# Kernel tuning notes

Hardware: AMD Instinct MI355X
Metric: run time of the kernel (lower is better)

The kernel has to match this reference:

```python
import jax, jax.numpy as jnp
import numpy as np

B, T, DIM, H, E, D, K = 2, 2048, 1024, 8, 5, 64, 3


def setup_inputs() -> dict:
    key = jax.random.key(0)
    ks = jax.random.split(key, 7)
    s = 0.02
    return {
        "x": jax.random.normal(ks[0], (B, T, DIM), dtype=jnp.float32),
        "w_q": jax.random.normal(ks[1], (DIM, H * E * D), dtype=jnp.float32) * s,
        "w_kv": jax.random.normal(ks[2], (DIM, 2 * H * E * D), dtype=jnp.float32) * s,
        "w_s": jax.random.normal(ks[3], (DIM, H * E), dtype=jnp.float32) * s,
        "w_d": jax.random.normal(ks[4], (DIM, H * E), dtype=jnp.float32) * s,
        "w_o_w": jax.random.normal(ks[5], (H, DIM, D), dtype=jnp.float32) * s,
        "w_o_b": jax.random.normal(ks[6], (H, DIM), dtype=jnp.float32) * s,
    }


def _select(proj_full, eps, s):
    # Faithful to torch scatter_(3, eps, s): value s[..., k] is written at
    # expert slot eps[..., k]; multiplying the full projection by that sparse
    # score tensor and summing over e == gather selected experts, weight by
    # the FIRST K raw scores (not the topk values), and sum.
    sel = jnp.take_along_axis(proj_full, eps[..., None], axis=3)  # b t h K d
    return (sel * s[..., :K, None]).sum(axis=3)  # b t h d


def reference(x, w_q, w_kv, w_s, w_d, w_o_w, w_o_b):
    scale = D ** (-0.5)
    ss = jax.nn.sigmoid(x @ w_s).reshape(B, T, H, E)
    sd = jax.nn.sigmoid(x @ w_d).reshape(B, T, H, E)
    eps_s = jax.lax.top_k(ss, K)[1]  # b t h K
    eps_d = jax.lax.top_k(sd, K)[1]

    q_full = (x @ w_q).reshape(B, T, H, E, D)
    q = _select(q_full, eps_d, sd)  # b t h d

    kv_full = (x @ w_kv).reshape(B, T, 2, H, E, D)
    k = _select(kv_full[:, :, 0], eps_s, ss)
    v = _select(kv_full[:, :, 1], eps_s, ss)

    attn = jnp.einsum("bihd,bjhd->bhij", q * scale, k)
    probs = jax.nn.softmax(attn, axis=-1)
    out = jnp.einsum("bhij,bjhd->bihd", probs, v)  # b t h d

    # per-head Linear(dim_head, dim) then sum over heads (stack+sum)
    return jnp.einsum("bihd,hfd->bif", out, w_o_w) + w_o_b.sum(axis=0)
```

## Files before the change

### kernel.cpp

```cpp
#include <hip/hip_runtime.h>

#define DEV __device__ __forceinline__

typedef float f32x4 __attribute__((ext_vector_type(4)));
typedef short s16x8 __attribute__((ext_vector_type(8)));
typedef unsigned short u16;
typedef unsigned int u32;

constexpr int Bb = 2, Tt = 2048, DIMc = 1024, Hh = 8, Ee = 5, Dd = 64;
constexpr int NTOK = Bb * Tt;
constexpr int NQ = Hh * Ee * Dd;

DEV u16 f2bf(float f) {
  union { float f; u32 u; } v; v.f = f;
  u32 r = v.u + 0x7fffu + ((v.u >> 16) & 1u);
  return (u16)(r >> 16);
}

DEV u32 pk2(float a, float b) {
  return (u32)f2bf(a) | ((u32)f2bf(b) << 16);
}

DEV s16x8 ld8(const u16* p) {
  uint4 u = *reinterpret_cast<const uint4*>(p);
  return __builtin_bit_cast(s16x8, u);
}

DEV f32x4 mfma16(s16x8 a, s16x8 b, f32x4 c) {
  return __builtin_amdgcn_mfma_f32_16x16x32_bf16(a, b, c, 0, 0, 0);
}

DEV void gld16(const void* g, void* l) {
  __builtin_amdgcn_global_load_lds(
      (const __attribute__((address_space(1))) void*)g,
      (__attribute__((address_space(3))) void*)l, 16, 0, 0);
}

__launch_bounds__(256)
__global__ void k_prep(const float* __restrict__ x, const float* __restrict__ wq,
                       const float* __restrict__ wkv, const float* __restrict__ wow,
                       const float* __restrict__ wob, const float* __restrict__ wsr,
                       const float* __restrict__ wdr,
                       u16* __restrict__ xb, u16* __restrict__ wT,
                       u16* __restrict__ woT, float* __restrict__ bsum,
                       float* __restrict__ wsdT) {
  int bid = blockIdx.x, t = threadIdx.x;
  if (bid < 4096) {
    int i = bid * 256 + t;
    float4 v = reinterpret_cast<const float4*>(x)[i];
    u16 r0 = f2bf(v.x), r1 = f2bf(v.y), r2 = f2bf(v.z), r3 = f2bf(v.w);
    u32 lo = (u32)r0 | ((u32)r1 << 16);
    u32 hi = (u32)r2 | ((u32)r3 << 16);
    reinterpret_cast<uint2*>(xb)[i] = make_uint2(lo, hi);
  } else if (bid < 11776) {
    int b2 = bid - 4096;
    int R0 = (b2 % 240) * 32;
    int C0 = (b2 / 240) * 32;
    int s = R0 / 2560, rem = R0 % 2560;
    int h = rem / 320, n0 = rem % 320;
    const float* src; int ld; int col0;
    if (s == 0) { src = wq;  ld = 2560; col0 = h * 320 + n0; }
    else        { src = wkv; ld = 5120; col0 = (s - 1) * 2560 + h * 320 + n0; }
    __shared__ float tile[32][33];
    int tx = t & 31, ty = t >> 5;
    #pragma unroll
    for (int i = 0; i < 4; i++) {
      int c = C0 + ty + 8 * i;
      tile[ty + 8 * i][tx] = src[(size_t)c * ld + col0 + tx];
    }
    __syncthreads();
    #pragma unroll
    for (int i = 0; i < 4; i++) {
      int n = ty + 8 * i;
      wT[(size_t)(R0 + n) * 1024 + C0 + tx] = f2bf(tile[tx][n]);
    }
  } else if (bid < 12032) {
    int b2 = bid - 11776;
    int f = b2 * 4 + (t >> 6), d = t & 63;
    #pragma unroll
    for (int h = 0; h < 8; h++)
      woT[(size_t)f * 512 + h * 64 + d] = f2bf(wow[((size_t)h * 1024 + f) * 64 + d]);
  } else if (bid < 12036) {
    int f = (bid - 12032) * 256 + t;
    float s = 0.f;
    #pragma unroll
    for (int h = 0; h < 8; h++) s += wob[h * 1024 + f];
    bsum[f] = s;
  } else {
    int j = bid - 12036;
    const float* src = (j < 40) ? wsr : wdr;
    int c = (j < 40) ? j : j - 40;
    for (int i = t; i < 1024; i += 256)
      wsdT[(size_t)j * 1024 + i] = src[(size_t)i * 40 + c];
  }
}

__launch_bounds__(320)
__global__ void k_scores(const float* __restrict__ x, const float* __restrict__ wsdT,
                         int* __restrict__ eps_s, int* __restrict__ eps_d,
                         float* __restrict__ ss3, float* __restrict__ sd3) {
  int tokb = blockIdx.x * 8;
  __shared__ float xl[8][1028];
  __shared__ float sc[8][80];
  const float4* xsrc = reinterpret_cast<const float4*>(x + (size_t)tokb * 1024);
  for (int i = threadIdx.x; i < 2048; i += 320) {
    int tok = i >> 8, col4 = i & 255;
    *reinterpret_cast<float4*>(&xl[tok][col4 * 4]) = xsrc[i];
  }
  __syncthreads();
  {
    int tok = threadIdx.x & 7, j = threadIdx.x >> 3;
    const float4* wsp = reinterpret_cast<const float4*>(wsdT + (size_t)j * 1024);
    const float4* wdp = reinterpret_cast<const float4*>(wsdT + (size_t)(j + 40) * 1024);
    float as0 = 0.f, as1 = 0.f, ad0 = 0.f, ad1 = 0.f;
    #pragma unroll 4
    for (int k4 = 0; k4 < 256; k4 += 2) {
      float4 x0 = *reinterpret_cast<const float4*>(&xl[tok][k4 * 4]);
      float4 x1 = *reinterpret_cast<const float4*>(&xl[tok][k4 * 4 + 4]);
      float4 wsv0 = wsp[k4], wsv1 = wsp[k4 + 1];
      float4 wdv0 = wdp[k4], wdv1 = wdp[k4 + 1];
      as0 += x0.x * wsv0.x + x0.y * wsv0.y + x0.z * wsv0.z + x0.w * wsv0.w;
      as1 += x1.x * wsv1.x + x1.y * wsv1.y + x1.z * wsv1.z + x1.w * wsv1.w;
      ad0 += x0.x * wdv0.x + x0.y * wdv0.y + x0.z * wdv0.z + x0.w * wdv0.w;
      ad1 += x1.x * wdv1.x + x1.y * wdv1.y + x1.z * wdv1.z + x1.w * wdv1.w;
    }
    float as = as0 + as1, ad = ad0 + ad1;
    sc[tok][j]      = 1.f / (1.f + expf(-as));
    sc[tok][40 + j] = 1.f / (1.f + expf(-ad));
  }
  __syncthreads();
  int t2 = threadIdx.x;
  if (t2 < 128) {
    int tt = t2 >> 4, u = t2 & 15, h = u >> 1, which = u & 1;
    const float* S = &sc[tt][which * 40 + h * 5];
    float v[5];
    #pragma unroll
    for (int e = 0; e < 5; e++) v[e] = S[e];
    int tok = tokb + tt;
    int base = (tok * 8 + h) * 3;
    int* eps = which ? eps_d : eps_s;
    float* w3 = which ? sd3 : ss3;
    bool used[5] = {false, false, false, false, false};
    #pragma unroll
    for (int kk = 0; kk < 3; kk++) {
      float best = -1e30f; int bi = 0;
      #pragma unroll
      for (int e = 0; e < 5; e++)
        if (!used[e] && v[e] > best) { best = v[e]; bi = e; }
      used[bi] = true;
      eps[base + kk] = bi;
    }
    #pragma unroll
    for (int kk = 0; kk < 3; kk++) w3[base + kk] = S[kk];
  }
}

__launch_bounds__(512)
__global__ void k_proj(const u16* __restrict__ xb, const u16* __restrict__ wT,
                       const int* __restrict__ eps_d, const int* __restrict__ eps_s,
                       const float* __restrict__ sd3, const float* __restrict__ ss3,
                       u16* __restrict__ qw, u16* __restrict__ kw, u16* __restrict__ vw) {
  int tok0 = blockIdx.x * 128;
  int h = blockIdx.y;
  int s = blockIdx.z;
  int Rbase = (s * 8 + h) * 320;
  __shared__ alignas(16) u16 bsA[128 * 64];
  __shared__ alignas(16) u16 bsB[320 * 64];
  int wv = threadIdx.x >> 6, l = threadIdx.x & 63;
  int g = l >> 4, c = l & 15;
  f32x4 acc[20];
  #pragma unroll
  for (int i = 0; i < 20; i++) acc[i] = (f32x4){0.f, 0.f, 0.f, 0.f};

  const u16* wTp0 = wT + (size_t)Rbase * 1024;
  const u16* xbp0 = xb + (size_t)tok0 * 1024;

  for (int k0 = 0; k0 < 1024; k0 += 64) {
    __syncthreads();
    const u16* wTp = wTp0 + k0;
    #pragma unroll
    for (int j = 0; j < 5; j++) {
      int ch = wv * 320 + j * 64 + l;
      int row = ch >> 3, part = ch & 7;
      gld16(wTp + (size_t)row * 1024 + ((part * 8) ^ ((row & 7) * 8)),
            &bsB[(wv * 320 + j * 64) * 8]);
    }
    const u16* xbp = xbp0 + k0;
    #pragma unroll
    for (int j = 0; j < 2; j++) {
      int ch = wv * 128 + j * 64 + l;
      int row = ch >> 3, part = ch & 7;
      gld16(xbp + (size_t)row * 1024 + ((part * 8) ^ ((row & 7) * 8)),
            &bsA[(wv * 128 + j * 64) * 8]);
    }
    __syncthreads();

    #pragma unroll
    for (int kk = 0; kk < 2; kk++) {
      int off = (kk * 32 + g * 8) ^ ((c & 7) * 8);
      s16x8 a = *reinterpret_cast<const s16x8*>(&bsA[(wv * 16 + c) * 64 + off]);
      #pragma unroll
      for (int nt = 0; nt < 20; nt++) {
        s16x8 b = *reinterpret_cast<const s16x8*>(&bsB[(nt * 16 + c) * 64 + off]);
        acc[nt] = mfma16(a, b, acc[nt]);
      }
    }
  }

  const int* eps = (s == 0) ? eps_d : eps_s;
  const float* w3 = (s == 0) ? sd3 : ss3;
  float scale = (s == 0) ? 0.125f : 1.0f;
  u16* dst = (s == 0) ? qw : (s == 1 ? kw : vw);
  #pragma unroll
  for (int r = 0; r < 4; r++) {
    int tokr = tok0 + wv * 16 + g * 4 + r;
    int base = (tokr * 8 + h) * 3;
    int e0 = eps[base], e1 = eps[base + 1], e2 = eps[base + 2];
    float w0 = w3[base], w1 = w3[base + 1], w2 = w3[base + 2];
    float we[5];
    #pragma unroll
    for (int e = 0; e < 5; e++)
      we[e] = (e0 == e ? w0 : 0.f) + (e1 == e ? w1 : 0.f) + (e2 == e ? w2 : 0.f);
    int b = tokr >> 11, t = tokr & 2047;
    size_t obase = (((size_t)b * 8 + h) * 2048 + t) * 64;
    #pragma unroll
    for (int dh = 0; dh < 4; dh++) {
      float vq = 0.f;
      #pragma unroll
      for (int e = 0; e < 5; e++) vq += we[e] * acc[e * 4 + dh][r];
      dst[obase + dh * 16 + c] = f2bf(vq * scale);
    }
  }
}

__global__ void k_trv(const u16* __restrict__ vw, u16* __restrict__ vT) {
  int bh = blockIdx.z;
  int t0 = blockIdx.x * 32, d0 = blockIdx.y * 32;
  __shared__ u16 tile[32][33];
  const u16* src = vw + (size_t)bh * 2048 * 64;
  u16* dst = vT + (size_t)bh * 64 * 2048;
  int tx = threadIdx.x, ty = threadIdx.y;
  #pragma unroll
  for (int i = 0; i < 4; i++)
    tile[ty + 8 * i][tx] = src[(size_t)(t0 + ty + 8 * i) * 64 + d0 + tx];
  __syncthreads();
  int p = 8 * ((tx & 15) >> 2) + (tx & 3) + ((tx >= 16) ? 4 : 0);
  #pragma unroll
  for (int i = 0; i < 4; i++)
    dst[(size_t)(d0 + ty + 8 * i) * 2048 + t0 + p] = tile[tx][ty + 8 * i];
}

__launch_bounds__(512)
__global__ void k_attn(const u16* __restrict__ qw, const u16* __restrict__ kw,
                       const u16* __restrict__ vT, u16* __restrict__ ow) {
  int bh = blockIdx.y;
  int b = bh >> 3, h = bh & 7;
  int q0 = blockIdx.x * 64;
  int wv = threadIdx.x >> 6, l = threadIdx.x & 63;
  int seg = wv >> 2, wq = wv & 3;
  int g = l >> 4, c = l & 15;
  const u16* qp = qw + (size_t)bh * 2048 * 64;
  const u16* kp = kw + (size_t)bh * 2048 * 64;
  const u16* vp = vT + (size_t)bh * 64 * 2048;
  __shared__ alignas(16) u16 Kl[2][128 * 64];
  __shared__ alignas(16) u16 Vl[2][64 * 128];

  s16x8 qa0 = ld8(qp + (size_t)(q0 + wq * 16 + c) * 64 + 0 + 8 * g);
  s16x8 qa1 = ld8(qp + (size_t)(q0 + wq * 16 + c) * 64 + 32 + 8 * g);

  f32x4 o[4];
  #pragma unroll
  for (int i = 0; i < 4; i++) o[i] = (f32x4){0.f, 0.f, 0.f, 0.f};
  float ssum = 0.f;

  const int kb0 = seg * 1024;
  for (int kt = 0; kt < 1024; kt += 128) {
    int kbase = kb0 + kt;
    __syncthreads();
    #pragma unroll
    for (int j = 0; j < 4; j++) {
      int ch = (wq * 4 + j) * 64 + l;
      int row = ch >> 3, sl = ch & 7;
      gld16(kp + (size_t)(kbase + row) * 64 + ((sl ^ (row & 7)) * 8),
            &Kl[seg][(wq * 4 + j) * 64 * 8]);
    }
    #pragma unroll
    for (int j = 0; j < 4; j++) {
      int ch = (wq * 4 + j) * 64 + l;
      int d = ch >> 4, sl = ch & 15;
      gld16(vp + (size_t)d * 2048 + kbase + ((sl ^ (d & 15)) * 8),
            &Vl[seg][(wq * 4 + j) * 64 * 8]);
    }
    __syncthreads();

    #pragma unroll
    for (int kk = 0; kk < 4; kk++) {
      int r0 = kk * 32 + c, r1 = kk * 32 + 16 + c;
      int c7 = c & 7;
      s16x8 ka0 = *reinterpret_cast<const s16x8*>(&Kl[seg][r0 * 64 + ((0 + g) ^ c7) * 8]);
      s16x8 ka1 = *reinterpret_cast<const s16x8*>(&Kl[seg][r0 * 64 + ((4 + g) ^ c7) * 8]);
      s16x8 kc0 = *reinterpret_cast<const s16x8*>(&Kl[seg][r1 * 64 + ((0 + g) ^ c7) * 8]);
      s16x8 kc1 = *reinterpret_cast<const s16x8*>(&Kl[seg][r1 * 64 + ((4 + g) ^ c7) * 8]);

      f32x4 s0 = (f32x4){0.f, 0.f, 0.f, 0.f};
      f32x4 s1 = (f32x4){0.f, 0.f, 0.f, 0.f};
      s0 = mfma16(ka0, qa0, s0);
      s0 = mfma16(ka1, qa1, s0);
      s1 = mfma16(kc0, qa0, s1);
      s1 = mfma16(kc1, qa1, s1);

      float p00 = __expf(s0[0]), p01 = __expf(s0[1]);
      float p02 = __expf(s0[2]), p03 = __expf(s0[3]);
      float p10 = __expf(s1[0]), p11 = __expf(s1[1]);
      float p12 = __expf(s1[2]), p13 = __expf(s1[3]);
      ssum += (p00 + p01) + (p02 + p03) + (p10 + p11) + (p12 + p13);

      uint4 pw = make_uint4(pk2(p00, p01), pk2(p02, p03),
                            pk2(p10, p11), pk2(p12, p13));
      s16x8 pa = __builtin_bit_cast(s16x8, pw);

      #pragma unroll
      for (int nt = 0; nt < 4; nt++) {
        int d = nt * 16 + c;
        s16x8 vb = *reinterpret_cast<const s16x8*>(&Vl[seg][d * 128 + (((kk * 4 + g) ^ (d & 15)) * 8)]);
        o[nt] = mfma16(pa, vb, o[nt]);
      }
    }
  }

  ssum += __shfl_xor(ssum, 16, 64);
  ssum += __shfl_xor(ssum, 32, 64);

  float* osp  = reinterpret_cast<float*>(&Kl[0][0]);
  float* sslp = reinterpret_cast<float*>(&Vl[0][0]);
  __syncthreads();
  if (g == 0) sslp[seg * 64 + wq * 16 + c] = ssum;
  if (seg == 1) {
    #pragma unroll
    for (int r = 0; r < 4; r++)
      #pragma unroll
      for (int nt = 0; nt < 4; nt++)
        osp[(wq * 16 + g * 4 + r) * 64 + nt * 16 + c] = o[nt][r];
  }
  __syncthreads();
  if (seg == 0) {
    #pragma unroll
    for (int r = 0; r < 4; r++) {
      int q = g * 4 + r;
      float sm = sslp[wq * 16 + q] + sslp[64 + wq * 16 + q];
      float inv = 1.f / sm;
      int t = q0 + wq * 16 + q;
      #pragma unroll
      for (int nt = 0; nt < 4; nt++) {
        float val = (o[nt][r] + osp[(wq * 16 + q) * 64 + nt * 16 + c]) * inv;
        ow[((size_t)(b * 2048 + t)) * 512 + h * 64 + nt * 16 + c] = f2bf(val);
      }
    }
  }
}

__launch_bounds__(512)
__global__ void k_oproj(const u16* __restrict__ ow, const u16* __restrict__ woT,
                        const float* __restrict__ biasum, float* __restrict__ out) {
  int t0 = blockIdx.x * 128, f0 = blockIdx.y * 64;
  int wv = threadIdx.x >> 6, l = threadIdx.x & 63;
  int g = l >> 4, c = l & 15;
  f32x4 acc[4];
  #pragma unroll
  for (int i = 0; i < 4; i++) acc[i] = (f32x4){0.f, 0.f, 0.f, 0.f};
  for (int k0 = 0; k0 < 512; k0 += 32) {
    s16x8 a = ld8(ow + (size_t)(t0 + wv * 16 + c) * 512 + k0 + 8 * g);
    #pragma unroll
    for (int nt = 0; nt < 4; nt++) {
      s16x8 bfr = ld8(woT + (size_t)(f0 + nt * 16 + c) * 512 + k0 + 8 * g);
      acc[nt] = mfma16(a, bfr, acc[nt]);
    }
  }
  #pragma unroll
  for (int r = 0; r < 4; r++) {
    int t = t0 + wv * 16 + g * 4 + r;
    #pragma unroll
    for (int nt = 0; nt < 4; nt++) {
      int f = f0 + nt * 16 + c;
      out[(size_t)t * 1024 + f] = acc[nt][r] + biasum[f];
    }
  }
}

extern "C" void kernel_launch(void* const* d_in, const int* in_sizes, int n_in,
                              void* d_out, int out_size, void* d_ws, size_t ws_size,
                              hipStream_t stream) {
  const float* x    = (const float*)d_in[0];
  const float* w_q  = (const float*)d_in[1];
  const float* w_kv = (const float*)d_in[2];
  const float* w_s  = (const float*)d_in[3];
  const float* w_d  = (const float*)d_in[4];
  const float* w_ow = (const float*)d_in[5];
  const float* w_ob = (const float*)d_in[6];
  float* out = (float*)d_out;

  char* ws = (char*)d_ws;
  size_t o = 0;
  u16* xb     = (u16*)(ws + o); o += (size_t)NTOK * DIMc * 2;
  u16* wT     = (u16*)(ws + o); o += (size_t)3 * NQ * DIMc * 2;
  u16* woT    = (u16*)(ws + o); o += (size_t)1024 * 512 * 2;
  float* bsum = (float*)(ws + o); o += 4096;
  float* wsdT = (float*)(ws + o); o += (size_t)80 * 1024 * 4;
  int* eps_s  = (int*)(ws + o); o += (size_t)NTOK * 8 * 3 * 4;
  int* eps_d  = (int*)(ws + o); o += (size_t)NTOK * 8 * 3 * 4;
  float* ss3  = (float*)(ws + o); o += (size_t)NTOK * 8 * 3 * 4;
  float* sd3  = (float*)(ws + o); o += (size_t)NTOK * 8 * 3 * 4;
  u16* qw     = (u16*)(ws + o); o += (size_t)NTOK * 512 * 2;
  u16* kw     = (u16*)(ws + o); o += (size_t)NTOK * 512 * 2;
  u16* vw     = (u16*)(ws + o); o += (size_t)NTOK * 512 * 2;
  u16* vTw    = (u16*)(ws + o); o += (size_t)NTOK * 512 * 2;
  u16* oww    = (u16*)(ws + o); o += (size_t)NTOK * 512 * 2;

  k_prep<<<12116, 256, 0, stream>>>(x, w_q, w_kv, w_ow, w_ob, w_s, w_d,
                                    xb, wT, woT, bsum, wsdT);
  k_scores<<<512, 320, 0, stream>>>(x, wsdT, eps_s, eps_d, ss3, sd3);
  k_proj<<<dim3(32, 8, 3), 512, 0, stream>>>(xb, wT, eps_d, eps_s, sd3, ss3, qw, kw, vw);
  k_trv<<<dim3(64, 2, 16), dim3(32, 8), 0, stream>>>(vw, vTw);
  k_attn<<<dim3(32, 16), 512, 0, stream>>>(qw, kw, vTw, oww);
  k_oproj<<<dim3(32, 16), 512, 0, stream>>>(oww, woT, bsum, out);
}
```

Baseline: 211.0 us.

## Double-buffer LDS tiles in projection GEMM to overlap loads with MFMA

The projection kernel now keeps two LDS buffers for the A and B tiles. It issues the async global-to-LDS loads for the next K-slice before computing on the current one, and uses a vmcnt wait so only the older loads must finish. The goal is to hide global load latency that was exposed by the old load-sync-compute loop. LDS use doubles to about 112KB per block, which can limit occupancy and depends on hand-counted vmcnt values being correct.

Result: no change. 214.3 us (+1.6%).

```diff
diff --git a/kernel.cpp b/kernel.cpp
--- a/kernel.cpp
+++ b/kernel.cpp
@@ -164,8 +164,8 @@
   int h = blockIdx.y;
   int s = blockIdx.z;
   int Rbase = (s * 8 + h) * 320;
-  __shared__ alignas(16) u16 bsA[128 * 64];
-  __shared__ alignas(16) u16 bsB[320 * 64];
+  __shared__ alignas(16) u16 bsA[2][128 * 64];
+  __shared__ alignas(16) u16 bsB[2][320 * 64];
   int wv = threadIdx.x >> 6, l = threadIdx.x & 63;
   int g = l >> 4, c = l & 15;
   f32x4 acc[20];
@@ -175,37 +175,56 @@
   const u16* wTp0 = wT + (size_t)Rbase * 1024;
   const u16* xbp0 = xb + (size_t)tok0 * 1024;
 
-  for (int k0 = 0; k0 < 1024; k0 += 64) {
-    __syncthreads();
-    const u16* wTp = wTp0 + k0;
-    #pragma unroll
-    for (int j = 0; j < 5; j++) {
-      int ch = wv * 320 + j * 64 + l;
-      int row = ch >> 3, part = ch & 7;
-      gld16(wTp + (size_t)row * 1024 + ((part * 8) ^ ((row & 7) * 8)),
-            &bsB[(wv * 320 + j * 64) * 8]);
-    }
-    const u16* xbp = xbp0 + k0;
-    #pragma unroll
-    for (int j = 0; j < 2; j++) {
-      int ch = wv * 128 + j * 64 + l;
-      int row = ch >> 3, part = ch & 7;
-      gld16(xbp + (size_t)row * 1024 + ((part * 8) ^ ((row & 7) * 8)),
-            &bsA[(wv * 128 + j * 64) * 8]);
-    }
-    __syncthreads();
-
-    #pragma unroll
-    for (int kk = 0; kk < 2; kk++) {
-      int off = (kk * 32 + g * 8) ^ ((c & 7) * 8);
-      s16x8 a = *reinterpret_cast<const s16x8*>(&bsA[(wv * 16 + c) * 64 + off]);
-      #pragma unroll
-      for (int nt = 0; nt < 20; nt++) {
-        s16x8 b = *reinterpret_cast<const s16x8*>(&bsB[(nt * 16 + c) * 64 + off]);
-        acc[nt] = mfma16(a, b, acc[nt]);
-      }
-    }
-  }
+#define STAGE(BUF, K0)                                                        \
+  {                                                                           \
+    const u16* wTp = wTp0 + (K0);                                             \
+    _Pragma("unroll")                                                         \
+    for (int j = 0; j < 5; j++) {                                             \
+      int ch = wv * 320 + j * 64 + l;                                         \
+      int row = ch >> 3, part = ch & 7;                                       \
+      gld16(wTp + (size_t)row * 1024 + ((part * 8) ^ ((row & 7) * 8)),        \
+            &bsB[BUF][(wv * 320 + j * 64) * 8]);                              \
+    }                                                                         \
+    const u16* xbp = xbp0 + (K0);                                             \
+    _Pragma("unroll")                                                         \
+    for (int j = 0; j < 2; j++) {                                             \
+      int ch = wv * 128 + j * 64 + l;                                         \
+      int row = ch >> 3, part = ch & 7;                                       \
+      gld16(xbp + (size_t)row * 1024 + ((part * 8) ^ ((row & 7) * 8)),        \
+            &bsA[BUF][(wv * 128 + j * 64) * 8]);                              \
+    }                                                                         \
+  }
+
+#define COMPUTE(BUF)                                                          \
+  {                                                                           \
+    _Pragma("unroll")                                                         \
+    for (int kk = 0; kk < 2; kk++) {                                          \
+      int off = (kk * 32 + g * 8) ^ ((c & 7) * 8);                            \
+      s16x8 a = *reinterpret_cast<const s16x8*>(&bsA[BUF][(wv * 16 + c) * 64 + off]); \
+      _Pragma("unroll")                                                       \
+      for (int nt = 0; nt < 20; nt++) {                                       \
+        s16x8 b = *reinterpret_cast<const s16x8*>(&bsB[BUF][(nt * 16 + c) * 64 + off]); \
+        acc[nt] = mfma16(a, b, acc[nt]);                                      \
+      }                                                                       \
+    }                                                                         \
+  }
+
+  STAGE(0, 0)
+  for (int t = 0; t < 15; ++t) {
+    STAGE((t + 1) & 1, (t + 1) * 64)
+    asm volatile("s_waitcnt vmcnt(7)" ::: "memory");
+    __builtin_amdgcn_s_barrier();
+    __builtin_amdgcn_sched_barrier(0);
+    COMPUTE(t & 1)
+    __builtin_amdgcn_sched_barrier(0);
+    __builtin_amdgcn_s_barrier();
+  }
+  asm volatile("s_waitcnt vmcnt(0)" ::: "memory");
+  __builtin_amdgcn_s_barrier();
+  __builtin_amdgcn_sched_barrier(0);
+  COMPUTE(1)
+#undef STAGE
+#undef COMPUTE
 
   const int* eps = (s == 0) ? eps_d : eps_s;
   const float* w3 = (s == 0) ? sd3 : ss3;
```
